# Kernel optimization log

Measured on AMD Instinct MI355X. Metric: run time of the kernel, lower is better.

Reference implementation:

```python
import jax, jax.numpy as jnp
import numpy as np

B, T, D, U, S = 128, 256, 256, 256, 3
GRID_SIZE, SPLINE_ORDER = 5, 3
COEFFS = GRID_SIZE + SPLINE_ORDER  # 8


def _grid():
    h = 2.0 / GRID_SIZE  # grid_range = (-1, 1)
    return -1.0 + h * jnp.arange(-SPLINE_ORDER, GRID_SIZE + SPLINE_ORDER + 1, dtype=jnp.float32)


def _b_splines(x, grid):
    # Cox-de Boor recursion. x: (B, D) -> (B, D, COEFFS)
    x = x[..., None]
    b = ((x >= grid[:-1]) & (x < grid[1:])).astype(x.dtype)
    for k in range(1, SPLINE_ORDER + 1):
        b = (x - grid[:-(k + 1)]) / (grid[k:-1] - grid[:-(k + 1)]) * b[..., :-1] \
          + (grid[k + 1:] - x) / (grid[k + 1:] - grid[1:-k]) * b[..., 1:]
    return b


def setup_inputs() -> dict:
    key = jax.random.key(0)
    ks = jax.random.split(key, 8)
    x = jax.random.normal(ks[0], (B, T, D), jnp.float32)
    kernel = jax.random.normal(ks[1], (D, 3 * U), jnp.float32) / np.float32(np.sqrt(D))
    recurrent_kernel = jax.random.normal(ks[2], (U, 3 * U), jnp.float32) / np.float32(np.sqrt(U))
    # unit_forget_bias: gate order (i, f, c)
    bias = jnp.zeros((3 * U,), jnp.float32).at[U:2 * U].set(1.0)
    sub_tkan_kernel = jax.random.normal(ks[3], (S, 2), jnp.float32)
    sub_tkan_recurrent_kernel = jax.random.normal(ks[4], (S, 2 * D), jnp.float32) / np.float32(np.sqrt(D))
    aggregated_weight = jax.random.normal(ks[5], (S, U), jnp.float32)
    aggregated_bias = jnp.zeros((U,), jnp.float32)
    kan_base_weight = jax.random.normal(ks[6], (S, D, 1), jnp.float32) / np.float32(np.sqrt(D))
    kan_spline_weight = jax.random.normal(ks[7], (S, D, COEFFS, 1), jnp.float32) * 0.1
    return dict(x=x, kernel=kernel, recurrent_kernel=recurrent_kernel, bias=bias,
                sub_tkan_kernel=sub_tkan_kernel,
                sub_tkan_recurrent_kernel=sub_tkan_recurrent_kernel,
                aggregated_weight=aggregated_weight, aggregated_bias=aggregated_bias,
                kan_base_weight=kan_base_weight, kan_spline_weight=kan_spline_weight)


def reference(x, kernel, recurrent_kernel, bias, sub_tkan_kernel,
              sub_tkan_recurrent_kernel, aggregated_weight, aggregated_bias,
              kan_base_weight, kan_spline_weight):
    grid = _grid()
    b, t, d = x.shape
    u = kernel.shape[1] // 3
    s = sub_tkan_kernel.shape[0]
    skx = sub_tkan_recurrent_kernel[:, :d]    # (S, D) input scale
    skh = sub_tkan_recurrent_kernel[:, d:]    # (S, D) sub-state scale
    srk_h = sub_tkan_kernel[:, 0][:, None, None]  # (S,1,1)
    srk_x = sub_tkan_kernel[:, 1][:, None, None]  # (S,1,1)

    def kan(xin, bw, sw):
        # xin (B, D), bw (D, 1), sw (D, COEFFS, 1) -> (B, 1)
        base = jax.nn.silu(xin) @ bw
        spline = jnp.einsum('bdc,dco->bo', _b_splines(xin, grid), sw)
        return base + spline

    kan_v = jax.vmap(kan)  # over the S sub-layers

    def step(carry, x_t):
        h, c, sub = carry  # (B,U), (B,U), (S,B,1)
        z = x_t @ kernel + h @ recurrent_kernel + bias  # (B, 3U)
        zi, zf, zc = jnp.split(z, 3, axis=1)
        i = jax.nn.sigmoid(zi)
        f = jax.nn.sigmoid(zf)
        c_new = f * c + i * jnp.tanh(zc)
        # KAN sub-layers: mix input with scalar sub-state, evaluate spline net
        agg_in = x_t[None] * skx[:, None, :] + sub * skh[:, None, :]  # (S,B,D)
        sub_out = kan_v(agg_in, kan_base_weight, kan_spline_weight)   # (S,B,1)
        sub_new = srk_h * sub_out + srk_x * sub                       # (S,B,1)
        # output gate from aggregated sub-layer outputs
        o = jax.nn.sigmoid(sub_out[..., 0].T @ aggregated_weight + aggregated_bias)  # (B,U)
        h_new = o * jnp.tanh(c_new)
        return (h_new, c_new, sub_new), h_new

    init = (jnp.zeros((b, u), x.dtype), jnp.zeros((b, u), x.dtype),
            jnp.zeros((s, b, 1), x.dtype))
    _, ys = jax.lax.scan(step, init, jnp.swapaxes(x, 0, 1))
    return jnp.swapaxes(ys, 0, 1)  # (B, T, U) full sequence of hidden states
```

## Files before the change

### kernel.cpp

```cpp
#include <hip/hip_runtime.h>

#define B_  128
#define T_  256
#define D_  256
#define U_  256
#define TU  768
#define TC  64
#define NC  (T_/TC)

__device__ __forceinline__ float sigm(float x) { return 1.f / (1.f + __expf(-x)); }

__device__ __forceinline__ float tanh_fast(float x) {
    float e = __expf(2.f * x);
    return 1.f - 2.f / (e + 1.f);
}

__device__ __forceinline__ float spline_eval(float x, const float* __restrict__ ksw_lds, int u) {
    float xc = (x + 2.2f) * 2.5f;
    float fj = floorf(xc);
    int   j  = (int)fj;
    float tl = xc - fj;
    float t2 = tl * tl, t3 = t2 * tl;
    float om = 1.f - tl;
    const float S = 1.f / 6.f;
    float w0 = om * om * om * S;
    float w1 = (3.f * t3 - 6.f * t2 + 4.f) * S;
    float w2 = (-3.f * t3 + 3.f * t2 + 3.f * tl + 1.f) * S;
    float w3 = t3 * S;
    bool  v  = (j >= 0) && (j <= 10);
    float r  = 0.f;
#pragma unroll
    for (int k = 0; k < 4; ++k) {
        int   m  = j - 3 + k;
        bool  ok = v && (m >= 0) && (m <= 7);
        int   mc = min(max(m, 0), 7);
        float wk = (k == 0) ? w0 : (k == 1) ? w1 : (k == 2) ? w2 : w3;
        float cf = ksw_lds[u * 9 + mc];
        r += ok ? wk * cf : 0.f;
    }
    return r;
}

__global__ void k0_init(float* __restrict__ wh, float* __restrict__ wc,
                        float* __restrict__ wsub, float* __restrict__ xh) {
    int i = blockIdx.x * 256 + threadIdx.x;
    wh[i] = 0.f;
    wc[i] = 0.f;
    ((int*)xh)[i]         = 1;
    ((int*)xh)[i + 32768] = 1;
    if (i < 3 * B_) wsub[i] = 0.f;
}

__global__ __launch_bounds__(256) void k1_gemm(const float* __restrict__ X,
                                               const float* __restrict__ Km,
                                               const float* __restrict__ bias,
                                               float* __restrict__ A, int t0) {
    __shared__ float Xs[16][68];
    __shared__ float Ks[16][68];
    const int bm  = blockIdx.x * 64;
    const int bn  = blockIdx.y * 64;
    const int tid = threadIdx.x;
    const int ty = tid >> 4, tx = tid & 15;

    const int lr  = tid >> 2;
    const int lk4 = (tid & 3) * 4;
    const int rr  = bm + lr;
    const int b   = rr >> 6;
    const int tl  = rr & 63;
    const float* xrow = X + (size_t)(b * T_ + t0 + tl) * D_;

    const int kr  = tid >> 4;
    const int kn4 = (tid & 15) * 4;

    float acc[4][4] = {};
    for (int kb = 0; kb < 256; kb += 16) {
        float4 xv = *(const float4*)(xrow + kb + lk4);
        Xs[lk4 + 0][lr] = xv.x;
        Xs[lk4 + 1][lr] = xv.y;
        Xs[lk4 + 2][lr] = xv.z;
        Xs[lk4 + 3][lr] = xv.w;
        *(float4*)&Ks[kr][kn4] = *(const float4*)(Km + (size_t)(kb + kr) * TU + bn + kn4);
        __syncthreads();
#pragma unroll
        for (int k = 0; k < 16; ++k) {
            float4 av = *(float4*)&Xs[k][ty * 4];
            float4 bv = *(float4*)&Ks[k][tx * 4];
            acc[0][0] += av.x * bv.x; acc[0][1] += av.x * bv.y; acc[0][2] += av.x * bv.z; acc[0][3] += av.x * bv.w;
            acc[1][0] += av.y * bv.x; acc[1][1] += av.y * bv.y; acc[1][2] += av.y * bv.z; acc[1][3] += av.y * bv.w;
            acc[2][0] += av.z * bv.x; acc[2][1] += av.z * bv.y; acc[2][2] += av.z * bv.z; acc[2][3] += av.z * bv.w;
            acc[3][0] += av.w * bv.x; acc[3][1] += av.w * bv.y; acc[3][2] += av.w * bv.z; acc[3][3] += av.w * bv.w;
        }
        __syncthreads();
    }
    float4 bv = *(const float4*)(bias + bn + tx * 4);
#pragma unroll
    for (int i = 0; i < 4; ++i) {
        float4 o;
        o.x = acc[i][0] + bv.x; o.y = acc[i][1] + bv.y;
        o.z = acc[i][2] + bv.z; o.w = acc[i][3] + bv.w;
        *(float4*)(A + (size_t)(bm + ty * 4 + i) * TU + bn + tx * 4) = o;
    }
}

__global__ __launch_bounds__(512, 2)
void k2_rec(const float* __restrict__ A,
            const float* __restrict__ X,
            const float* __restrict__ R,
            const float* __restrict__ stk,
            const float* __restrict__ strk,
            const float* __restrict__ aggw,
            const float* __restrict__ aggb,
            const float* __restrict__ kbw,
            const float* __restrict__ ksw,
            float* __restrict__ out,
            float* __restrict__ ws_h,
            float* __restrict__ ws_c,
            float* __restrict__ ws_sub,
            float* __restrict__ xh,
            int t0) {
    __shared__ float hs[256];
    __shared__ float xs[256];
    __shared__ float zred[8][64][3];
    __shared__ float kred[768];
    __shared__ float so_l[3];
    __shared__ float subs[3];
    __shared__ float st2[6];
    __shared__ float hhist[TC][128];
    __shared__ float ksw_lds[768 * 9];

    const int tid  = threadIdx.x;
    const int lane = tid & 63;
    const int w    = tid >> 6;
    const int p    = w & 3;
    const int c    = ((w >> 2) << 6) | lane;
    const int b    = blockIdx.x & 127;
    const int r    = blockIdx.x >> 7;
    const int ui   = r * 128 + c;
    const bool pstate = (p == 0);

    float Rf[3][64];
#pragma unroll
    for (int g = 0; g < 3; ++g)
#pragma unroll
        for (int uu = 0; uu < 64; ++uu)
            Rf[g][uu] = R[(size_t)(p * 64 + uu) * TU + g * 256 + ui];

    const int s0 = tid >> 8, d0 = tid & 255;
    const float skx0 = strk[s0 * 512 + d0];
    const float skh0 = strk[s0 * 512 + 256 + d0];
    const float bw0  = kbw[tid];
    int u1i = -1;
    if (tid >= 64 && tid < 256)       u1i = tid - 64;
    else if (tid >= 320 && tid < 384) u1i = tid - 128;
    float skx1 = 0.f, skh1 = 0.f, bw1 = 0.f;
    if (u1i >= 0) {
        skx1 = strk[2 * 512 + u1i];
        skh1 = strk[2 * 512 + 256 + u1i];
        bw1  = kbw[512 + u1i];
    }

    const float aw0 = aggw[ui], aw1 = aggw[256 + ui], aw2 = aggw[512 + ui], ab = aggb[ui];
    float c_reg = ws_c[b * 256 + ui];

    for (int i = tid; i < 768 * 8; i += 512) ksw_lds[(i >> 3) * 9 + (i & 7)] = ksw[i];
    if (tid < 256) hs[tid] = ws_h[b * 256 + tid];
    if (tid < 256) xs[tid] = X[((size_t)b * T_ + t0) * D_ + tid];
    if (tid < 3)   subs[tid] = ws_sub[b * 3 + tid];
    if (tid < 6)   st2[tid] = stk[tid];

    float az0 = 0.f, az1 = 0.f, az2 = 0.f;
    float xv = 0.f;
    __syncthreads();

    for (int tl = 0; tl < TC; ++tl) {
        const int t = t0 + tl;

        if (pstate) {
            if (tl > 0) {
                float z0 = az0, z1 = az1, z2 = az2;
#pragma unroll
                for (int q = 0; q < 4; ++q) {
                    z0 += zred[w + q][lane][0];
                    z1 += zred[w + q][lane][1];
                    z2 += zred[w + q][lane][2];
                }
                float ig = sigm(z0);
                float fg = sigm(z1);
                c_reg = fg * c_reg + ig * tanh_fast(z2);
                float og = sigm(so_l[0] * aw0 + so_l[1] * aw1 + so_l[2] * aw2 + ab);
                float hn = og * tanh_fast(c_reg);
                hs[ui] = hn;
                hhist[tl - 1][c] = hn;
                unsigned hb = (__float_as_uint(hn) & ~1u) | (unsigned)(((t - 1) >> 1) & 1);
                __hip_atomic_store((unsigned*)&xh[((size_t)b * 2 + ((t - 1) & 1)) * 256 + ui],
                                   hb, __ATOMIC_RELAXED, __HIP_MEMORY_SCOPE_SYSTEM);
            }
            const float* Ap = A + ((size_t)b * TC + tl) * TU + ui;
            az0 = Ap[0]; az1 = Ap[256]; az2 = Ap[512];
        }
        if (u1i >= 0) {
            int tn = (t + 1 < T_) ? t + 1 : t;
            xv = X[((size_t)b * T_ + tn) * D_ + u1i];
        }
        {
            float a0 = xs[d0] * skx0 + subs[s0] * skh0;
            kred[tid] = a0 * sigm(a0) * bw0 + spline_eval(a0, ksw_lds, tid);
        }
        if (u1i >= 0) {
            float a1 = xs[u1i] * skx1 + subs[2] * skh1;
            kred[512 + u1i] = a1 * sigm(a1) * bw1 + spline_eval(a1, ksw_lds, 512 + u1i);
        }
        if (tl > 0 && tid >= 384) {
            const int uidx = (1 - r) * 128 + (tid - 384);
            const unsigned expect = (unsigned)(((t - 1) >> 1) & 1);
            const unsigned* src = (const unsigned*)&xh[((size_t)b * 2 + ((t - 1) & 1)) * 256 + uidx];
            unsigned v;
            do {
                v = __hip_atomic_load(src, __ATOMIC_RELAXED, __HIP_MEMORY_SCOPE_SYSTEM);
            } while ((v & 1u) != expect);
            hs[uidx] = __uint_as_float(v);
        }
        __syncthreads();

        {
            const float* hp = &hs[p * 64];
            float a0 = 0.f, a1 = 0.f, a2 = 0.f;
#pragma unroll
            for (int j = 0; j < 16; ++j) {
                float4 h4 = *(const float4*)(hp + j * 4);
                a0 = fmaf(h4.x, Rf[0][j * 4 + 0], a0);
                a1 = fmaf(h4.x, Rf[1][j * 4 + 0], a1);
                a2 = fmaf(h4.x, Rf[2][j * 4 + 0], a2);
                a0 = fmaf(h4.y, Rf[0][j * 4 + 1], a0);
                a1 = fmaf(h4.y, Rf[1][j * 4 + 1], a1);
                a2 = fmaf(h4.y, Rf[2][j * 4 + 1], a2);
                a0 = fmaf(h4.z, Rf[0][j * 4 + 2], a0);
                a1 = fmaf(h4.z, Rf[1][j * 4 + 2], a1);
                a2 = fmaf(h4.z, Rf[2][j * 4 + 2], a2);
                a0 = fmaf(h4.w, Rf[0][j * 4 + 3], a0);
                a1 = fmaf(h4.w, Rf[1][j * 4 + 3], a1);
                a2 = fmaf(h4.w, Rf[2][j * 4 + 3], a2);
            }
            zred[w][lane][0] = a0;
            zred[w][lane][1] = a1;
            zred[w][lane][2] = a2;
        }
        if (w < 3) {
            float v = kred[w * 256 + lane] + kred[w * 256 + 64 + lane]
                    + kred[w * 256 + 128 + lane] + kred[w * 256 + 192 + lane];
#pragma unroll
            for (int m = 32; m > 0; m >>= 1) v += __shfl_xor(v, m, 64);
            if (lane == 0) {
                so_l[w] = v;
                subs[w] = st2[w * 2] * v + st2[w * 2 + 1] * subs[w];
            }
        }
        if (u1i >= 0) xs[u1i] = xv;
        __syncthreads();
    }

    if (pstate) {
        float z0 = az0, z1 = az1, z2 = az2;
#pragma unroll
        for (int q = 0; q < 4; ++q) {
            z0 += zred[w + q][lane][0];
            z1 += zred[w + q][lane][1];
            z2 += zred[w + q][lane][2];
        }
        float ig = sigm(z0);
        float fg = sigm(z1);
        c_reg = fg * c_reg + ig * tanh_fast(z2);
        float og = sigm(so_l[0] * aw0 + so_l[1] * aw1 + so_l[2] * aw2 + ab);
        float hn = og * tanh_fast(c_reg);
        hhist[TC - 1][c] = hn;
        ws_h[b * 256 + ui] = hn;
        ws_c[b * 256 + ui] = c_reg;
        {
            const int s = t0 + TC - 1;
            unsigned hb = (__float_as_uint(hn) & ~1u) | (unsigned)(((s) >> 1) & 1);
            __hip_atomic_store((unsigned*)&xh[((size_t)b * 2 + (s & 1)) * 256 + ui],
                               hb, __ATOMIC_RELAXED, __HIP_MEMORY_SCOPE_SYSTEM);
        }
    }
    __syncthreads();
    for (int i = tid; i < TC * 128; i += 512) {
        int tl = i >> 7, cc = i & 127;
        out[((size_t)b * T_ + t0 + tl) * U_ + r * 128 + cc] = hhist[tl][cc];
    }
    if (tid < 3) ws_sub[b * 3 + tid] = subs[tid];
}

extern "C" void kernel_launch(void* const* d_in, const int* in_sizes, int n_in,
                              void* d_out, int out_size, void* d_ws, size_t ws_size,
                              hipStream_t stream) {
    const float* x    = (const float*)d_in[0];
    const float* Kmat = (const float*)d_in[1];
    const float* R    = (const float*)d_in[2];
    const float* bias = (const float*)d_in[3];
    const float* stk  = (const float*)d_in[4];
    const float* strk = (const float*)d_in[5];
    const float* aggw = (const float*)d_in[6];
    const float* aggb = (const float*)d_in[7];
    const float* kbw  = (const float*)d_in[8];
    const float* ksw  = (const float*)d_in[9];
    float* out = (float*)d_out;

    float* ws   = (float*)d_ws;
    float* A    = ws;
    float* wh   = A + (size_t)B_ * TC * TU;
    float* wc   = wh + B_ * U_;
    float* wsub = wc + B_ * U_;
    float* xh   = wsub + 512;

    k0_init<<<dim3(B_), dim3(256), 0, stream>>>(wh, wc, wsub, xh);
    for (int ci = 0; ci < NC; ++ci) {
        k1_gemm<<<dim3((B_ * TC) / 64, TU / 64), dim3(256), 0, stream>>>(x, Kmat, bias, A, ci * TC);
        k2_rec<<<dim3(2 * B_), dim3(512), 0, stream>>>(A, x, R, stk, strk, aggw, aggb, kbw, ksw,
                                                       out, wh, wc, wsub, xh, ci * TC);
    }
}
```

Baseline: 802.1 us.

## Widen input-projection GEMM tile to 64x128 and double-buffer LDS tiles

The chunked input-projection GEMM now gives each block a 64x128 output tile, so each thread computes a 4x8 accumulator tile. It double-buffers the X and K shared-memory tiles, prefetching the next k-slice into registers during compute, which leaves one barrier per k-step instead of two. The aim is more FMA work per LDS load and hiding global load latency. It costs more registers and LDS per block and halves the grid's column dimension, which reduces the number of blocks.

```diff
diff --git a/kernel.cpp b/kernel.cpp
--- a/kernel.cpp
+++ b/kernel.cpp
@@ -55,50 +55,77 @@
                                                const float* __restrict__ Km,
                                                const float* __restrict__ bias,
                                                float* __restrict__ A, int t0) {
-    __shared__ float Xs[16][68];
-    __shared__ float Ks[16][68];
+    __shared__ float Xs[2][16][68];
+    __shared__ float Ks[2][16][132];
+    const int tid = threadIdx.x;
     const int bm  = blockIdx.x * 64;
-    const int bn  = blockIdx.y * 64;
-    const int tid = threadIdx.x;
+    const int bn  = blockIdx.y * 128;
+
     const int ty = tid >> 4, tx = tid & 15;
-
-    const int lr  = tid >> 2;
-    const int lk4 = (tid & 3) * 4;
-    const int rr  = bm + lr;
-    const int b   = rr >> 6;
-    const int tl  = rr & 63;
-    const float* xrow = X + (size_t)(b * T_ + t0 + tl) * D_;
-
-    const int kr  = tid >> 4;
-    const int kn4 = (tid & 15) * 4;
-
-    float acc[4][4] = {};
-    for (int kb = 0; kb < 256; kb += 16) {
-        float4 xv = *(const float4*)(xrow + kb + lk4);
-        Xs[lk4 + 0][lr] = xv.x;
-        Xs[lk4 + 1][lr] = xv.y;
-        Xs[lk4 + 2][lr] = xv.z;
-        Xs[lk4 + 3][lr] = xv.w;
-        *(float4*)&Ks[kr][kn4] = *(const float4*)(Km + (size_t)(kb + kr) * TU + bn + kn4);
-        __syncthreads();
+    const int m0 = ty * 4, n0 = tx * 4;
+
+    const int xr = tid & 63, kq = (tid >> 6) * 4;
+    const int rr = bm + xr;
+    const float* xrow = X + (size_t)((rr >> 6) * T_ + t0 + (rr & 63)) * D_;
+
+    const int kr = tid >> 4, nq = (tid & 15) * 8;
+    const float* krow = Km + (size_t)kr * TU + bn + nq;
+
+    {
+        float4 xv  = *(const float4*)(xrow + kq);
+        float4 kv0 = *(const float4*)(krow);
+        float4 kv1 = *(const float4*)(krow + 4);
+        Xs[0][kq + 0][xr] = xv.x; Xs[0][kq + 1][xr] = xv.y;
+        Xs[0][kq + 2][xr] = xv.z; Xs[0][kq + 3][xr] = xv.w;
+        *(float4*)&Ks[0][kr][nq]     = kv0;
+        *(float4*)&Ks[0][kr][nq + 4] = kv1;
+    }
+    __syncthreads();
+
+    float acc[4][8] = {};
+    for (int kb = 0; kb < 16; ++kb) {
+        const int cur = kb & 1;
+        float4 xv, kv0, kv1;
+        if (kb + 1 < 16) {
+            const float* xp = xrow + (kb + 1) * 16 + kq;
+            const float* kp = krow + (size_t)(kb + 1) * 16 * TU;
+            xv  = *(const float4*)(xp);
+            kv0 = *(const float4*)(kp);
+            kv1 = *(const float4*)(kp + 4);
+        }
 #pragma unroll
         for (int k = 0; k < 16; ++k) {
-            float4 av = *(float4*)&Xs[k][ty * 4];
-            float4 bv = *(float4*)&Ks[k][tx * 4];
-            acc[0][0] += av.x * bv.x; acc[0][1] += av.x * bv.y; acc[0][2] += av.x * bv.z; acc[0][3] += av.x * bv.w;
-            acc[1][0] += av.y * bv.x; acc[1][1] += av.y * bv.y; acc[1][2] += av.y * bv.z; acc[1][3] += av.y * bv.w;
-            acc[2][0] += av.z * bv.x; acc[2][1] += av.z * bv.y; acc[2][2] += av.z * bv.z; acc[2][3] += av.z * bv.w;
-            acc[3][0] += av.w * bv.x; acc[3][1] += av.w * bv.y; acc[3][2] += av.w * bv.z; acc[3][3] += av.w * bv.w;
-        }
-        __syncthreads();
-    }
-    float4 bv = *(const float4*)(bias + bn + tx * 4);
+            float4 av = *(float4*)&Xs[cur][k][m0];
+            float4 b0 = *(float4*)&Ks[cur][k][n0];
+            float4 b1 = *(float4*)&Ks[cur][k][64 + n0];
+            float a[4]  = {av.x, av.y, av.z, av.w};
+            float bb[8] = {b0.x, b0.y, b0.z, b0.w, b1.x, b1.y, b1.z, b1.w};
+#pragma unroll
+            for (int i = 0; i < 4; ++i)
+#pragma unroll
+                for (int j = 0; j < 8; ++j)
+                    acc[i][j] = fmaf(a[i], bb[j], acc[i][j]);
+        }
+        if (kb + 1 < 16) {
+            const int nxt = cur ^ 1;
+            Xs[nxt][kq + 0][xr] = xv.x; Xs[nxt][kq + 1][xr] = xv.y;
+            Xs[nxt][kq + 2][xr] = xv.z; Xs[nxt][kq + 3][xr] = xv.w;
+            *(float4*)&Ks[nxt][kr][nq]     = kv0;
+            *(float4*)&Ks[nxt][kr][nq + 4] = kv1;
+            __syncthreads();
+        }
+    }
+    float4 bv0 = *(const float4*)(bias + bn + n0);
+    float4 bv1 = *(const float4*)(bias + bn + 64 + n0);
 #pragma unroll
     for (int i = 0; i < 4; ++i) {
-        float4 o;
-        o.x = acc[i][0] + bv.x; o.y = acc[i][1] + bv.y;
-        o.z = acc[i][2] + bv.z; o.w = acc[i][3] + bv.w;
-        *(float4*)(A + (size_t)(bm + ty * 4 + i) * TU + bn + tx * 4) = o;
+        float4 o0, o1;
+        o0.x = acc[i][0] + bv0.x; o0.y = acc[i][1] + bv0.y;
+        o0.z = acc[i][2] + bv0.z; o0.w = acc[i][3] + bv0.w;
+        o1.x = acc[i][4] + bv1.x; o1.y = acc[i][5] + bv1.y;
+        o1.z = acc[i][6] + bv1.z; o1.w = acc[i][7] + bv1.w;
+        *(float4*)(A + (size_t)(bm + m0 + i) * TU + bn + n0)      = o0;
+        *(float4*)(A + (size_t)(bm + m0 + i) * TU + bn + 64 + n0) = o1;
     }
 }
 
@@ -314,7 +341,7 @@
 
     k0_init<<<dim3(B_), dim3(256), 0, stream>>>(wh, wc, wsub, xh);
     for (int ci = 0; ci < NC; ++ci) {
-        k1_gemm<<<dim3((B_ * TC) / 64, TU / 64), dim3(256), 0, stream>>>(x, Kmat, bias, A, ci * TC);
+        k1_gemm<<<dim3((B_ * TC) / 64, TU / 128), dim3(256), 0, stream>>>(x, Kmat, bias, A, ci * TC);
         k2_rec<<<dim3(2 * B_), dim3(512), 0, stream>>>(A, x, R, stk, strk, aggw, aggb, kbw, ksw,
                                                        out, wh, wc, wsub, xh, ci * TC);
     }
```

After: 789.1 us. Within noise of the previous version (-1.6%).
